# Performance work log

Measured on AMD Instinct MI355X. Metric: run time of the kernel, lower is better.

The kernel has to match this reference:

```python
import jax, jax.numpy as jnp
import numpy as np

H, HKV, D, HID = 32, 8, 128, 4096
EPS = 1e-6
ROPE_BASE = 10000.0
SCALE = D ** -0.5


def setup_inputs() -> dict:
    key = jax.random.key(0)
    ks = jax.random.split(key, 4)
    T = 2048
    x = jax.random.normal(ks[0], (T, HID), dtype=jnp.float32)
    w_qkv = jax.random.normal(ks[1], ((H + 2 * HKV) * D, HID), dtype=jnp.float32) * (HID ** -0.5)
    b_qkv = jax.random.normal(ks[2], ((H + 2 * HKV) * D,), dtype=jnp.float32) * 0.02
    q_norm_w = jnp.ones((D,), dtype=jnp.float32)
    k_norm_w = jnp.ones((D,), dtype=jnp.float32)
    w_o = jax.random.normal(ks[3], (HID, H * D), dtype=jnp.float32) * ((H * D) ** -0.5)
    return {"x": x, "w_qkv": w_qkv, "b_qkv": b_qkv, "q_norm_w": q_norm_w,
            "k_norm_w": k_norm_w, "w_o": w_o}


def _rms_norm(t, w):
    # per-head RMSNorm over the last (head_dim) axis
    var = jnp.mean(t * t, axis=-1, keepdims=True)
    return t * jax.lax.rsqrt(var + EPS) * w


def _rope(t, cos, sin):
    # neox-style half rotation; cos/sin: [T, D//2], t: [T, h, D]
    t1, t2 = jnp.split(t, 2, axis=-1)
    c = cos[:, None, :]
    s = sin[:, None, :]
    return jnp.concatenate([t1 * c - t2 * s, t2 * c + t1 * s], axis=-1)


def reference(x, w_qkv, b_qkv, q_norm_w, k_norm_w, w_o):
    T = x.shape[0]
    qkv = x @ w_qkv.T + b_qkv                      # [T, (H+2*HKV)*D]
    q, k, v = jnp.split(qkv, [H * D, (H + HKV) * D], axis=-1)
    q = q.reshape(T, H, D)
    k = k.reshape(T, HKV, D)
    v = v.reshape(T, HKV, D)

    # QK RMSNorm
    q = _rms_norm(q, q_norm_w)
    k = _rms_norm(k, k_norm_w)

    # rotary embedding, base 10000, full head_dim
    pos = jnp.arange(T, dtype=jnp.float32)
    inv_freq = 1.0 / (ROPE_BASE ** (jnp.arange(0, D, 2, dtype=jnp.float32) / D))
    freqs = pos[:, None] * inv_freq[None, :]        # [T, D//2]
    cos, sin = jnp.cos(freqs), jnp.sin(freqs)
    q = _rope(q, cos, sin)
    k = _rope(k, cos, sin)

    # GQA: kv_head_mapping = arange(HKV).repeat_interleave(H // HKV)
    groups = H // HKV
    k = jnp.repeat(k, groups, axis=1)               # [T, H, D]
    v = jnp.repeat(v, groups, axis=1)

    scores = jnp.einsum('thd,shd->hts', q, k) * SCALE   # [H, T, T]
    causal = jnp.tril(jnp.ones((T, T), dtype=bool))
    scores = jnp.where(causal[None], scores, jnp.finfo(scores.dtype).min)
    probs = jax.nn.softmax(scores, axis=-1)
    out = jnp.einsum('hts,shd->thd', probs, v)      # [T, H, D]
    return out.reshape(T, H * D) @ w_o.T            # [T, HID]
```

## Files before the change

### kernel.cpp

```cpp
#include <hip/hip_runtime.h>
#include <stdint.h>
#include <stddef.h>

typedef __bf16 bf16_t;
typedef __bf16 bf16x8 __attribute__((ext_vector_type(8)));
typedef float  f32x4  __attribute__((ext_vector_type(4)));

#define T_SEQ 2048
#define NH    32
#define NKV   8
#define DH    128
#define HIDN  4096
#define NQKV  6144
#define SCALE 0.08838834764831845f

__device__ inline float b2f(bf16_t v) {
  uint32_t u = ((uint32_t)__builtin_bit_cast(uint16_t, v)) << 16;
  return __builtin_bit_cast(float, u);
}
__device__ inline bf16_t f2b(float f) {
  uint32_t u = __builtin_bit_cast(uint32_t, f);
  u = (u + 0x7fffu + ((u >> 16) & 1u)) >> 16;
  return __builtin_bit_cast(bf16_t, (uint16_t)u);
}
__device__ inline void gl_lds16(const void* g, void* l) {
  __builtin_amdgcn_global_load_lds(
      (__attribute__((address_space(1))) void*)g,
      (__attribute__((address_space(3))) void*)l, 16, 0, 0);
}
__device__ inline f32x4 mfma16(bf16x8 a, bf16x8 b, f32x4 c) {
  return __builtin_amdgcn_mfma_f32_16x16x32_bf16(a, b, c, 0, 0, 0);
}
__device__ inline void store_val(float* p, float v)  { *p = v; }
__device__ inline void store_val(bf16_t* p, float v) { *p = f2b(v); }

__global__ __launch_bounds__(256)
void cvt_f32_bf16(const float* __restrict__ src, bf16_t* __restrict__ dst) {
  const size_t i = ((size_t)blockIdx.x * 256 + threadIdx.x) * 8;
  float4 a = *(const float4*)(src + i);
  float4 b = *(const float4*)(src + i + 4);
  bf16x8 o;
  o[0] = f2b(a.x); o[1] = f2b(a.y); o[2] = f2b(a.z); o[3] = f2b(a.w);
  o[4] = f2b(b.x); o[5] = f2b(b.y); o[6] = f2b(b.z); o[7] = f2b(b.w);
  *(bf16x8*)(dst + i) = o;
}

template <bool BIAS, typename TOUT>
__global__ __launch_bounds__(256)
void gemm_bt(const bf16_t* __restrict__ A, const bf16_t* __restrict__ Bw,
             const float* __restrict__ bias, TOUT* __restrict__ C,
             int M, int N, int K) {
  __shared__ __align__(16) char smem[32768];
  char* sA = smem;
  char* sB = smem + 16384;
  const int tid  = threadIdx.x;
  const int lane = tid & 63, wave = tid >> 6;
  const int quad = lane >> 4, l16 = lane & 15;
  const int wm = wave >> 1, wn = wave & 1;
  const int m0 = blockIdx.y * 128, n0 = blockIdx.x * 128;

  f32x4 acc[4][4] = {};
  const int kTiles = K >> 6;

  for (int kt = 0; kt < kTiles; ++kt) {
    const int kb = kt << 6;
    __syncthreads();
#pragma unroll
    for (int i = 0; i < 4; ++i) {
      int p = i * 256 + tid;
      int row = p >> 3, gc = (p & 7) ^ (row & 7);
      gl_lds16(A  + (size_t)(m0 + row) * K + kb + gc * 8, sA + p * 16);
      gl_lds16(Bw + (size_t)(n0 + row) * K + kb + gc * 8, sB + p * 16);
    }
    __syncthreads();
#pragma unroll
    for (int ks = 0; ks < 2; ++ks) {
      bf16x8 af[4], bfr[4];
      const int c = ks * 4 + quad;
#pragma unroll
      for (int i = 0; i < 4; ++i) {
        int ra = wm * 64 + i * 16 + l16;
        af[i]  = *(const bf16x8*)(sA + ra * 128 + ((c ^ (ra & 7)) * 16));
        int rb = wn * 64 + i * 16 + l16;
        bfr[i] = *(const bf16x8*)(sB + rb * 128 + ((c ^ (rb & 7)) * 16));
      }
#pragma unroll
      for (int i = 0; i < 4; ++i)
#pragma unroll
        for (int j = 0; j < 4; ++j)
          acc[i][j] = mfma16(af[i], bfr[j], acc[i][j]);
    }
  }
#pragma unroll
  for (int i = 0; i < 4; ++i) {
    int mrow = m0 + wm * 64 + i * 16 + quad * 4;
#pragma unroll
    for (int j = 0; j < 4; ++j) {
      int ncol = n0 + wn * 64 + j * 16 + l16;
      float bv = BIAS ? bias[ncol] : 0.f;
#pragma unroll
      for (int r = 0; r < 4; ++r)
        store_val(&C[(size_t)(mrow + r) * N + ncol], acc[i][j][r] + bv);
    }
  }
}

__global__ __launch_bounds__(256)
void prep_kernel(const bf16_t* __restrict__ qkv, const float* __restrict__ qw,
                 const float* __restrict__ kw, bf16_t* __restrict__ Qp,
                 bf16_t* __restrict__ Kp, bf16_t* __restrict__ Vp) {
  const int id   = blockIdx.x * 4 + (threadIdx.x >> 6);
  const int lane = threadIdx.x & 63;
  const int t = id / 48, slot = id % 48;
  const bf16_t* src = qkv + (size_t)t * NQKV + slot * DH;
  float x1 = b2f(src[lane]), x2 = b2f(src[lane + 64]);
  float o1, o2;
  if (slot < 40) {
    float ssq = x1 * x1 + x2 * x2;
#pragma unroll
    for (int m = 1; m < 64; m <<= 1) ssq += __shfl_xor(ssq, m, 64);
    float rms = rsqrtf(ssq * (1.f / 128.f) + 1e-6f);
    const float* w = (slot < 32) ? qw : kw;
    float n1 = x1 * rms * w[lane];
    float n2 = x2 * rms * w[lane + 64];
    float inv = exp2f(-0.20762050593046014f * (float)lane);
    float ang = (float)t * inv;
    float cs = cosf(ang), sn = sinf(ang);
    o1 = n1 * cs - n2 * sn;
    o2 = n2 * cs + n1 * sn;
  } else { o1 = x1; o2 = x2; }
  bf16_t* dst;
  if (slot < 32)      dst = Qp + ((size_t)t * NH  + slot)        * DH;
  else if (slot < 40) dst = Kp + ((size_t)t * NKV + (slot - 32)) * DH;
  else                dst = Vp + ((size_t)t * NKV + (slot - 40)) * DH;
  dst[lane] = f2b(o1); dst[lane + 64] = f2b(o2);
}

__global__ __launch_bounds__(256)
void vtrans_kernel(const bf16_t* __restrict__ Vp, bf16_t* __restrict__ Vt) {
  __shared__ bf16_t tile[64 * 66];
  const int t0 = blockIdx.x * 64, d0 = blockIdx.y * 64, kvh = blockIdx.z;
  const int tid = threadIdx.x;
#pragma unroll
  for (int i = 0; i < 2; ++i) {
    int id = i * 256 + tid;
    int tr = id >> 3, dc = id & 7;
    bf16x8 v = *(const bf16x8*)(Vp + ((size_t)(t0 + tr) * NKV + kvh) * DH + d0 + dc * 8);
#pragma unroll
    for (int e = 0; e < 8; ++e) tile[tr * 66 + dc * 8 + e] = v[e];
  }
  __syncthreads();
#pragma unroll
  for (int i = 0; i < 2; ++i) {
    int id = i * 256 + tid;
    int dr = id >> 3, tc = id & 7;
    bf16x8 o;
#pragma unroll
    for (int e = 0; e < 8; ++e) o[e] = tile[(tc * 8 + e) * 66 + dr];
    *(bf16x8*)(Vt + ((size_t)kvh * DH + d0 + dr) * T_SEQ + t0 + tc * 8) = o;
  }
}

__global__ __launch_bounds__(256)
void attn_kernel(const bf16_t* __restrict__ Qp, const bf16_t* __restrict__ Kp,
                 const bf16_t* __restrict__ Vt, bf16_t* __restrict__ Out) {
  __shared__ __align__(16) char smem[40960];
  char* sK  = smem;
  char* sVT = smem + 16384;
  char* sP  = smem + 32768;
  const int tid  = threadIdx.x;
  const int lane = tid & 63, wave = tid >> 6;
  const int quad = lane >> 4, l16 = lane & 15;
  const int b = blockIdx.x, h = blockIdx.y;
  const int qt_lo = b, qt_hi = 31 - b;
  const int kvh = h >> 2;

  bf16x8 qf_lo[4], qf_hi[4];
  {
    const int row_lo = qt_lo * 64 + wave * 16 + l16;
    const int row_hi = qt_hi * 64 + wave * 16 + l16;
#pragma unroll
    for (int ks = 0; ks < 4; ++ks) {
      qf_lo[ks] = *(const bf16x8*)(Qp + ((size_t)row_lo * NH + h) * DH + ks * 32 + quad * 8);
      qf_hi[ks] = *(const bf16x8*)(Qp + ((size_t)row_hi * NH + h) * DH + ks * 32 + quad * 8);
    }
  }
  f32x4 acc_lo[8] = {}, acc_hi[8] = {};
  float m_lo[4], l_lo[4], m_hi[4], l_hi[4];
#pragma unroll
  for (int r = 0; r < 4; ++r) {
    m_lo[r] = -3e38f; l_lo[r] = 0.f; m_hi[r] = -3e38f; l_hi[r] = 0.f;
  }

  char* sPw = sP + wave * 2048;

  auto compute = [&](bf16x8 (&qf)[4], f32x4 (&acc)[8], float (&mrow)[4],
                     float (&lrow)[4], int qt, int kt) {
    f32x4 sfr[4] = {};
#pragma unroll
    for (int ks = 0; ks < 4; ++ks) {
      const int c = ks * 4 + quad;
#pragma unroll
      for (int j = 0; j < 4; ++j) {
        int row = j * 16 + l16;
        bf16x8 kf = *(const bf16x8*)(sK + row * 256 + ((c ^ (row & 15)) * 16));
        sfr[j] = mfma16(qf[ks], kf, sfr[j]);
      }
    }
    float sv[4][4];
    const bool diag = (kt == qt);
#pragma unroll
    for (int j = 0; j < 4; ++j)
#pragma unroll
      for (int r = 0; r < 4; ++r) {
        float s = sfr[j][r] * SCALE;
        if (diag) {
          int qg = wave * 16 + quad * 4 + r;
          int kg = j * 16 + l16;
          if (kg > qg) s = -3e38f;
        }
        sv[j][r] = s;
      }
#pragma unroll
    for (int r = 0; r < 4; ++r) {
      float mx = fmaxf(fmaxf(sv[0][r], sv[1][r]), fmaxf(sv[2][r], sv[3][r]));
#pragma unroll
      for (int m = 1; m < 16; m <<= 1) mx = fmaxf(mx, __shfl_xor(mx, m, 64));
      float mnew  = fmaxf(mrow[r], mx);
      float alpha = __expf(mrow[r] - mnew);
      float rs = 0.f;
#pragma unroll
      for (int j = 0; j < 4; ++j) {
        float p = __expf(sv[j][r] - mnew);
        sv[j][r] = p;
        rs += p;
      }
#pragma unroll
      for (int m = 1; m < 16; m <<= 1) rs += __shfl_xor(rs, m, 64);
      lrow[r] = lrow[r] * alpha + rs;
      mrow[r] = mnew;
#pragma unroll
      for (int j2 = 0; j2 < 8; ++j2) acc[j2][r] *= alpha;
    }
#pragma unroll
    for (int j = 0; j < 4; ++j)
#pragma unroll
      for (int r = 0; r < 4; ++r) {
        int prow = quad * 4 + r;
        int col  = j * 16 + l16;
        int c    = col >> 3;
        ((bf16_t*)(sPw + prow * 128 + ((c ^ (prow & 7)) * 16)))[col & 7] = f2b(sv[j][r]);
      }
    __asm__ volatile("" ::: "memory");
    bf16x8 pf[2];
#pragma unroll
    for (int ks2 = 0; ks2 < 2; ++ks2) {
      int c = ks2 * 4 + quad;
      pf[ks2] = *(const bf16x8*)(sPw + l16 * 128 + ((c ^ (l16 & 7)) * 16));
    }
    __asm__ volatile("" ::: "memory");
#pragma unroll
    for (int j2 = 0; j2 < 8; ++j2)
#pragma unroll
      for (int ks2 = 0; ks2 < 2; ++ks2) {
        int d = j2 * 16 + l16;
        int c = ks2 * 4 + quad;
        bf16x8 vf = *(const bf16x8*)(sVT + d * 128 + ((c ^ (d & 7)) * 16));
        acc[j2] = mfma16(pf[ks2], vf, acc[j2]);
      }
  };

  for (int kt = 0; kt <= qt_hi; ++kt) {
    const int k0 = kt * 64;
    __syncthreads();
#pragma unroll
    for (int i = 0; i < 4; ++i) {
      int p = i * 256 + tid;
      int row = p >> 4, gc = (p & 15) ^ (row & 15);
      gl_lds16(Kp + ((size_t)(k0 + row) * NKV + kvh) * DH + gc * 8, sK + p * 16);
    }
#pragma unroll
    for (int i = 0; i < 4; ++i) {
      int p = i * 256 + tid;
      int d = p >> 3, gc = (p & 7) ^ (d & 7);
      gl_lds16(Vt + ((size_t)kvh * DH + d) * T_SEQ + k0 + gc * 8, sVT + p * 16);
    }
    __syncthreads();
    compute(qf_hi, acc_hi, m_hi, l_hi, qt_hi, kt);
    if (kt <= qt_lo)
      compute(qf_lo, acc_lo, m_lo, l_lo, qt_lo, kt);
  }

#pragma unroll
  for (int r = 0; r < 4; ++r) {
    float inv_h = 1.f / l_hi[r], inv_l = 1.f / l_lo[r];
    int qg_h = qt_hi * 64 + wave * 16 + quad * 4 + r;
    int qg_l = qt_lo * 64 + wave * 16 + quad * 4 + r;
#pragma unroll
    for (int j2 = 0; j2 < 8; ++j2) {
      int d = j2 * 16 + l16;
      Out[(size_t)qg_h * (NH * DH) + h * DH + d] = f2b(acc_hi[j2][r] * inv_h);
      Out[(size_t)qg_l * (NH * DH) + h * DH + d] = f2b(acc_lo[j2][r] * inv_l);
    }
  }
}

extern "C" void kernel_launch(void* const* d_in, const int* in_sizes, int n_in,
                              void* d_out, int out_size, void* d_ws, size_t ws_size,
                              hipStream_t stream) {
  const float* x    = (const float*)d_in[0];
  const float* wqkv = (const float*)d_in[1];
  const float* bqkv = (const float*)d_in[2];
  const float* qnw  = (const float*)d_in[3];
  const float* knw  = (const float*)d_in[4];
  const float* wo   = (const float*)d_in[5];
  float* out = (float*)d_out;

  char* ws = (char*)d_ws;
  bf16_t* xb    = (bf16_t*)(ws);
  bf16_t* wqkvb = (bf16_t*)(ws + 16777216);
  bf16_t* wob   = (bf16_t*)(ws);
  bf16_t* qkv   = (bf16_t*)(ws + 67108864);
  bf16_t* At    = (bf16_t*)(ws + 67108864);
  bf16_t* Qp    = (bf16_t*)(ws + 92274688);
  bf16_t* Kp    = (bf16_t*)(ws + 109051904);
  bf16_t* Vp    = (bf16_t*)(ws + 113246208);
  bf16_t* Vt    = (bf16_t*)(ws + 117440512);

  cvt_f32_bf16<<<(2048 * 4096) / 2048, 256, 0, stream>>>(x, xb);
  cvt_f32_bf16<<<(6144 * 4096) / 2048, 256, 0, stream>>>(wqkv, wqkvb);
  gemm_bt<true, bf16_t><<<dim3(NQKV / 128, T_SEQ / 128), 256, 0, stream>>>(
      xb, wqkvb, bqkv, qkv, T_SEQ, NQKV, HIDN);
  prep_kernel<<<(T_SEQ * 48) / 4, 256, 0, stream>>>(qkv, qnw, knw, Qp, Kp, Vp);
  vtrans_kernel<<<dim3(T_SEQ / 64, DH / 64, NKV), 256, 0, stream>>>(Vp, Vt);
  attn_kernel<<<dim3(16, NH), 256, 0, stream>>>(Qp, Kp, Vt, At);
  cvt_f32_bf16<<<(4096 * 4096) / 2048, 256, 0, stream>>>(wo, wob);
  gemm_bt<false, float><<<dim3(HIDN / 128, T_SEQ / 128), 256, 0, stream>>>(
      At, wob, nullptr, out, T_SEQ, HIDN, HIDN);
}
```

Before: 605.4 us.

## Register-prefetch GEMM tiles and interleave dual query tiles in attention

The GEMM now loads the next K tile from global memory into registers while the current tile is computed, then writes it to LDS, replacing direct global-to-LDS loads with a software prefetch. The attention kernel merges the two per-block query-tile computations so each K and V fragment read from LDS feeds both the hi and lo tiles. It also gives each tile its own P scratch buffer, which needs more shared memory. Both changes aim to raise MFMA overlap and cut LDS traffic, at the cost of more registers and LDS that may lower occupancy.

Measured after the change: 652.7 us. 1.08x slower.

```diff
diff --git a/kernel.cpp b/kernel.cpp
--- a/kernel.cpp
+++ b/kernel.cpp
@@ -59,20 +59,32 @@
   const int wm = wave >> 1, wn = wave & 1;
   const int m0 = blockIdx.y * 128, n0 = blockIdx.x * 128;
 
-  f32x4 acc[4][4] = {};
-  const int kTiles = K >> 6;
-
-  for (int kt = 0; kt < kTiles; ++kt) {
-    const int kb = kt << 6;
-    __syncthreads();
+  bf16x8 rA[4], rB[4];
+  auto load_tile = [&](int kb) {
 #pragma unroll
     for (int i = 0; i < 4; ++i) {
       int p = i * 256 + tid;
       int row = p >> 3, gc = (p & 7) ^ (row & 7);
-      gl_lds16(A  + (size_t)(m0 + row) * K + kb + gc * 8, sA + p * 16);
-      gl_lds16(Bw + (size_t)(n0 + row) * K + kb + gc * 8, sB + p * 16);
-    }
+      rA[i] = *(const bf16x8*)(A  + (size_t)(m0 + row) * K + kb + gc * 8);
+      rB[i] = *(const bf16x8*)(Bw + (size_t)(n0 + row) * K + kb + gc * 8);
+    }
+  };
+
+  f32x4 acc[4][4] = {};
+  const int kTiles = K >> 6;
+  load_tile(0);
+
+  for (int kt = 0; kt < kTiles; ++kt) {
     __syncthreads();
+#pragma unroll
+    for (int i = 0; i < 4; ++i) {
+      int p = i * 256 + tid;
+      *(bf16x8*)(sA + p * 16) = rA[i];
+      *(bf16x8*)(sB + p * 16) = rB[i];
+    }
+    __syncthreads();
+    if (kt + 1 < kTiles) load_tile((kt + 1) << 6);
+
 #pragma unroll
     for (int ks = 0; ks < 2; ++ks) {
       bf16x8 af[4], bfr[4];
@@ -164,7 +176,7 @@
 __global__ __launch_bounds__(256)
 void attn_kernel(const bf16_t* __restrict__ Qp, const bf16_t* __restrict__ Kp,
                  const bf16_t* __restrict__ Vt, bf16_t* __restrict__ Out) {
-  __shared__ __align__(16) char smem[40960];
+  __shared__ __align__(16) char smem[49152];
   char* sK  = smem;
   char* sVT = smem + 16384;
   char* sP  = smem + 32768;
@@ -192,21 +204,11 @@
     m_lo[r] = -3e38f; l_lo[r] = 0.f; m_hi[r] = -3e38f; l_hi[r] = 0.f;
   }
 
-  char* sPw = sP + wave * 2048;
-
-  auto compute = [&](bf16x8 (&qf)[4], f32x4 (&acc)[8], float (&mrow)[4],
-                     float (&lrow)[4], int qt, int kt) {
-    f32x4 sfr[4] = {};
-#pragma unroll
-    for (int ks = 0; ks < 4; ++ks) {
-      const int c = ks * 4 + quad;
-#pragma unroll
-      for (int j = 0; j < 4; ++j) {
-        int row = j * 16 + l16;
-        bf16x8 kf = *(const bf16x8*)(sK + row * 256 + ((c ^ (row & 15)) * 16));
-        sfr[j] = mfma16(qf[ks], kf, sfr[j]);
-      }
-    }
+  char* sP_hi = sP + wave * 2048;
+  char* sP_lo = sP + 8192 + wave * 2048;
+
+  auto softmax_p = [&](f32x4 (&sfr)[4], f32x4 (&acc)[8], float (&mrow)[4],
+                       float (&lrow)[4], int qt, int kt, char* sPw) {
     float sv[4][4];
     const bool diag = (kt == qt);
 #pragma unroll
@@ -251,12 +253,48 @@
         int c    = col >> 3;
         ((bf16_t*)(sPw + prow * 128 + ((c ^ (prow & 7)) * 16)))[col & 7] = f2b(sv[j][r]);
       }
+  };
+
+  for (int kt = 0; kt <= qt_hi; ++kt) {
+    const int k0 = kt * 64;
+    const bool dual = (kt <= qt_lo);
+    __syncthreads();
+#pragma unroll
+    for (int i = 0; i < 4; ++i) {
+      int p = i * 256 + tid;
+      int row = p >> 4, gc = (p & 15) ^ (row & 15);
+      gl_lds16(Kp + ((size_t)(k0 + row) * NKV + kvh) * DH + gc * 8, sK + p * 16);
+    }
+#pragma unroll
+    for (int i = 0; i < 4; ++i) {
+      int p = i * 256 + tid;
+      int d = p >> 3, gc = (p & 7) ^ (d & 7);
+      gl_lds16(Vt + ((size_t)kvh * DH + d) * T_SEQ + k0 + gc * 8, sVT + p * 16);
+    }
+    __syncthreads();
+
+    f32x4 s_hi[4] = {}, s_lo[4] = {};
+#pragma unroll
+    for (int ks = 0; ks < 4; ++ks) {
+      const int c = ks * 4 + quad;
+#pragma unroll
+      for (int j = 0; j < 4; ++j) {
+        int row = j * 16 + l16;
+        bf16x8 kf = *(const bf16x8*)(sK + row * 256 + ((c ^ (row & 15)) * 16));
+        s_hi[j] = mfma16(qf_hi[ks], kf, s_hi[j]);
+        if (dual) s_lo[j] = mfma16(qf_lo[ks], kf, s_lo[j]);
+      }
+    }
+    softmax_p(s_hi, acc_hi, m_hi, l_hi, qt_hi, kt, sP_hi);
+    if (dual) softmax_p(s_lo, acc_lo, m_lo, l_lo, qt_lo, kt, sP_lo);
     __asm__ volatile("" ::: "memory");
-    bf16x8 pf[2];
+    bf16x8 pf_hi[2], pf_lo[2];
 #pragma unroll
     for (int ks2 = 0; ks2 < 2; ++ks2) {
       int c = ks2 * 4 + quad;
-      pf[ks2] = *(const bf16x8*)(sPw + l16 * 128 + ((c ^ (l16 & 7)) * 16));
+      int off = l16 * 128 + ((c ^ (l16 & 7)) * 16);
+      pf_hi[ks2] = *(const bf16x8*)(sP_hi + off);
+      if (dual) pf_lo[ks2] = *(const bf16x8*)(sP_lo + off);
     }
     __asm__ volatile("" ::: "memory");
 #pragma unroll
@@ -266,29 +304,9 @@
         int d = j2 * 16 + l16;
         int c = ks2 * 4 + quad;
         bf16x8 vf = *(const bf16x8*)(sVT + d * 128 + ((c ^ (d & 7)) * 16));
-        acc[j2] = mfma16(pf[ks2], vf, acc[j2]);
-      }
-  };
-
-  for (int kt = 0; kt <= qt_hi; ++kt) {
-    const int k0 = kt * 64;
-    __syncthreads();
-#pragma unroll
-    for (int i = 0; i < 4; ++i) {
-      int p = i * 256 + tid;
-      int row = p >> 4, gc = (p & 15) ^ (row & 15);
-      gl_lds16(Kp + ((size_t)(k0 + row) * NKV + kvh) * DH + gc * 8, sK + p * 16);
-    }
-#pragma unroll
-    for (int i = 0; i < 4; ++i) {
-      int p = i * 256 + tid;
-      int d = p >> 3, gc = (p & 7) ^ (d & 7);
-      gl_lds16(Vt + ((size_t)kvh * DH + d) * T_SEQ + k0 + gc * 8, sVT + p * 16);
-    }
-    __syncthreads();
-    compute(qf_hi, acc_hi, m_hi, l_hi, qt_hi, kt);
-    if (kt <= qt_lo)
-      compute(qf_lo, acc_lo, m_lo, l_lo, qt_lo, kt);
+        acc_hi[j2] = mfma16(pf_hi[ks2], vf, acc_hi[j2]);
+        if (dual) acc_lo[j2] = mfma16(pf_lo[ks2], vf, acc_lo[j2]);
+      }
   }
 
 #pragma unroll
```

## Double-buffer attention K/V tiles and register-prefetch GEMM tiles

Applied to the files above, without the earlier changes.

The attention kernel now keeps two LDS buffers for K and V^T. It issues the next tile's async global-to-LDS loads right after the barrier, so they overlap with compute on the current tile, and it needs only one barrier per iteration. The GEMM drops direct global-to-LDS loads in favour of prefetching the next k-tile into registers while the current tile is computed, then storing those registers into LDS. The cost is more LDS per attention block (72KB), which may limit occupancy, and more registers in the GEMM.

After: 593.7 us. About the same (-1.9%).

```diff
diff --git a/kernel.cpp b/kernel.cpp
--- a/kernel.cpp
+++ b/kernel.cpp
@@ -59,20 +59,32 @@
   const int wm = wave >> 1, wn = wave & 1;
   const int m0 = blockIdx.y * 128, n0 = blockIdx.x * 128;
 
-  f32x4 acc[4][4] = {};
-  const int kTiles = K >> 6;
-
-  for (int kt = 0; kt < kTiles; ++kt) {
-    const int kb = kt << 6;
-    __syncthreads();
+  bf16x8 rA[4], rB[4];
+  auto load_tile = [&](int kb) {
 #pragma unroll
     for (int i = 0; i < 4; ++i) {
       int p = i * 256 + tid;
       int row = p >> 3, gc = (p & 7) ^ (row & 7);
-      gl_lds16(A  + (size_t)(m0 + row) * K + kb + gc * 8, sA + p * 16);
-      gl_lds16(Bw + (size_t)(n0 + row) * K + kb + gc * 8, sB + p * 16);
-    }
+      rA[i] = *(const bf16x8*)(A  + (size_t)(m0 + row) * K + kb + gc * 8);
+      rB[i] = *(const bf16x8*)(Bw + (size_t)(n0 + row) * K + kb + gc * 8);
+    }
+  };
+
+  f32x4 acc[4][4] = {};
+  const int kTiles = K >> 6;
+  load_tile(0);
+
+  for (int kt = 0; kt < kTiles; ++kt) {
     __syncthreads();
+#pragma unroll
+    for (int i = 0; i < 4; ++i) {
+      int p = i * 256 + tid;
+      *(bf16x8*)(sA + p * 16) = rA[i];
+      *(bf16x8*)(sB + p * 16) = rB[i];
+    }
+    __syncthreads();
+    if (kt + 1 < kTiles) load_tile((kt + 1) << 6);
+
 #pragma unroll
     for (int ks = 0; ks < 2; ++ks) {
       bf16x8 af[4], bfr[4];
@@ -164,16 +176,14 @@
 __global__ __launch_bounds__(256)
 void attn_kernel(const bf16_t* __restrict__ Qp, const bf16_t* __restrict__ Kp,
                  const bf16_t* __restrict__ Vt, bf16_t* __restrict__ Out) {
-  __shared__ __align__(16) char smem[40960];
-  char* sK  = smem;
-  char* sVT = smem + 16384;
-  char* sP  = smem + 32768;
+  __shared__ __align__(16) char smem[73728];
   const int tid  = threadIdx.x;
   const int lane = tid & 63, wave = tid >> 6;
   const int quad = lane >> 4, l16 = lane & 15;
   const int b = blockIdx.x, h = blockIdx.y;
   const int qt_lo = b, qt_hi = 31 - b;
   const int kvh = h >> 2;
+  char* sPw = smem + 65536 + wave * 2048;
 
   bf16x8 qf_lo[4], qf_hi[4];
   {
@@ -192,10 +202,26 @@
     m_lo[r] = -3e38f; l_lo[r] = 0.f; m_hi[r] = -3e38f; l_hi[r] = 0.f;
   }
 
-  char* sPw = sP + wave * 2048;
-
-  auto compute = [&](bf16x8 (&qf)[4], f32x4 (&acc)[8], float (&mrow)[4],
-                     float (&lrow)[4], int qt, int kt) {
+  auto stage = [&](int kt) {
+    char* sK = smem + (kt & 1) * 16384;
+    char* sV = smem + 32768 + (kt & 1) * 16384;
+    const int k0 = kt * 64;
+#pragma unroll
+    for (int i = 0; i < 4; ++i) {
+      int p = i * 256 + tid;
+      int row = p >> 4, gc = (p & 15) ^ (row & 15);
+      gl_lds16(Kp + ((size_t)(k0 + row) * NKV + kvh) * DH + gc * 8, sK + p * 16);
+    }
+#pragma unroll
+    for (int i = 0; i < 4; ++i) {
+      int p = i * 256 + tid;
+      int d = p >> 3, gc = (p & 7) ^ (d & 7);
+      gl_lds16(Vt + ((size_t)kvh * DH + d) * T_SEQ + k0 + gc * 8, sV + p * 16);
+    }
+  };
+
+  auto compute = [&](const bf16x8 (&qf)[4], f32x4 (&acc)[8], float (&mrow)[4],
+                     float (&lrow)[4], int qt, int kt, char* sK, char* sVT) {
     f32x4 sfr[4] = {};
 #pragma unroll
     for (int ks = 0; ks < 4; ++ks) {
@@ -270,25 +296,15 @@
       }
   };
 
+  stage(0);
   for (int kt = 0; kt <= qt_hi; ++kt) {
-    const int k0 = kt * 64;
     __syncthreads();
-#pragma unroll
-    for (int i = 0; i < 4; ++i) {
-      int p = i * 256 + tid;
-      int row = p >> 4, gc = (p & 15) ^ (row & 15);
-      gl_lds16(Kp + ((size_t)(k0 + row) * NKV + kvh) * DH + gc * 8, sK + p * 16);
-    }
-#pragma unroll
-    for (int i = 0; i < 4; ++i) {
-      int p = i * 256 + tid;
-      int d = p >> 3, gc = (p & 7) ^ (d & 7);
-      gl_lds16(Vt + ((size_t)kvh * DH + d) * T_SEQ + k0 + gc * 8, sVT + p * 16);
-    }
-    __syncthreads();
-    compute(qf_hi, acc_hi, m_hi, l_hi, qt_hi, kt);
+    if (kt < qt_hi) stage(kt + 1);
+    char* sK  = smem + (kt & 1) * 16384;
+    char* sVT = smem + 32768 + (kt & 1) * 16384;
+    compute(qf_hi, acc_hi, m_hi, l_hi, qt_hi, kt, sK, sVT);
     if (kt <= qt_lo)
-      compute(qf_lo, acc_lo, m_lo, l_lo, qt_lo, kt);
+      compute(qf_lo, acc_lo, m_lo, l_lo, qt_lo, kt, sK, sVT);
   }
 
 #pragma unroll
```
